# Performance work log

Measured on AMD Instinct MI355X. Metric: run time of the kernel, lower is better.

Reference implementation:

```python
import jax, jax.numpy as jnp
import numpy as np

SIGMA_DIS = 3.0  # from __init__ default sigma_dis=3
PRED_SCALE = 3e-6  # keep sqrt-norms below sigma so max(sigma - d, 0) is not saturated at 0


def setup_inputs() -> dict:
    key = jax.random.key(0)
    k1, k2 = jax.random.split(key)
    C, H, W = 8, 2048, 2048
    K = 32  # number of connected kernel components (labels 1..K, 0 = background)
    pred = jax.random.normal(k1, (C, H, W), dtype=jnp.float32) * PRED_SCALE
    kernel_labels = jax.random.randint(k2, (H, W), 0, K + 1, dtype=jnp.int32)
    regions_mask = jnp.ones((H, W), dtype=bool)  # unused by the original forward
    return {
        "pred_similarities": pred,
        "regions_mask": regions_mask,
        "kernel_labels": kernel_labels,
        "num_kernel": K,
    }


def _l_dis(pred, labels_flat, num_kernel, sigma):
    # pred: [C, H, W]; labels_flat: [H*W] int, values in 0..num_kernel (0 = background).
    C = pred.shape[0]
    flat = pred.reshape(C, -1).T  # [P, C]
    # Per-kernel, per-channel masked sums (the Gk broadcast values): S[k, c]
    S = jax.ops.segment_sum(flat, labels_flat, num_segments=num_kernel + 1)  # [K+1, C]
    # Per-kernel pixel counts N[k]
    N = jax.ops.segment_sum(jnp.ones_like(labels_flat, dtype=pred.dtype),
                            labels_flat, num_segments=num_kernel + 1)  # [K+1]
    # Gk_i has value S[i,c] on kernel i's pixels and 0 elsewhere; supports of distinct
    # kernels are disjoint, so ||Gk_i - Gk_j||_F^2 = N[i]*sum_c S[i,c]^2 + N[j]*sum_c S[j,c]^2.
    A = (N * jnp.sum(S * S, axis=1))[1:]  # [K], drop background label 0
    pair_sq = A[:, None] + A[None, :]  # [K, K]
    D = jnp.maximum(sigma - jnp.sqrt(pair_sq), 0.0)
    term = jnp.log(D * D + 1.0)
    upper = jnp.triu(jnp.ones((num_kernel, num_kernel), dtype=bool), k=1)  # i<j pairs
    L = jnp.sum(jnp.where(upper, term, 0.0))
    scale = (num_kernel - 1) / num_kernel  # 1.0/num_kernel * (num_kernel - 1)
    return L * jnp.asarray(scale, pred.dtype)


def reference(pred_similarities, regions_mask, kernel_labels, num_kernel):
    # regions_mask is accepted but unused, matching the original forward.
    labels_flat = kernel_labels.reshape(-1)
    return _l_dis(pred_similarities, labels_flat, num_kernel, SIGMA_DIS)
```

## Files before the change

kernel.cpp:

```cpp
#include <hip/hip_runtime.h>
#include <hip/hip_bf16.h>
#include <math.h>


typedef __attribute__((ext_vector_type(8))) short short8;
typedef __attribute__((ext_vector_type(4))) float f32x4;

constexpr int NSEGF = 32;
constexpr int RPS   = 9;
constexpr int NROWS = NSEGF * RPS;
constexpr int BLK   = 256;
constexpr int WPB   = 4;
constexpr int NBLK  = 1024;
constexpr int NWAVES= NBLK * WPB;
constexpr int TPX   = 128;
constexpr int L1BLK = 32;
constexpr int SLABS = NBLK / L1BLK;
constexpr int L1BASE   = 1024;
constexpr int PARTBASE = 16384;

#define SCHED_FENCE asm volatile("" ::: "memory")
#define WAITVM(n)   asm volatile("s_waitcnt vmcnt(" #n ")" ::: "memory")

typedef __attribute__((address_space(1))) void A1v;
typedef __attribute__((address_space(3))) void A3v;

__device__ __forceinline__ void gload16(const void* g, void* l) {
  __builtin_amdgcn_global_load_lds((const A1v*)g, (A3v*)l, 16, 0, 0);
}

__device__ __forceinline__ short f2bf(float f) {
  return (short)__bfloat16_as_ushort(__float2bfloat16(f));
}

__device__ __forceinline__ float wave_sum64(float x) {
  int t;
  t = __builtin_amdgcn_update_dpp(0, __float_as_int(x), 0x111, 0xf, 0xf, true); x += __int_as_float(t);
  t = __builtin_amdgcn_update_dpp(0, __float_as_int(x), 0x112, 0xf, 0xf, true); x += __int_as_float(t);
  t = __builtin_amdgcn_update_dpp(0, __float_as_int(x), 0x114, 0xf, 0xf, true); x += __int_as_float(t);
  t = __builtin_amdgcn_update_dpp(0, __float_as_int(x), 0x118, 0xf, 0xf, true); x += __int_as_float(t);
  t = __builtin_amdgcn_update_dpp(0, __float_as_int(x), 0x142, 0xf, 0xf, true); x += __int_as_float(t);
  t = __builtin_amdgcn_update_dpp(0, __float_as_int(x), 0x143, 0xf, 0xf, true); x += __int_as_float(t);
  return x;
}

__device__ __forceinline__ void stage_pred(const float* __restrict__ pred,
                                           float* predbuf,
                                           size_t px0, int lane, size_t P) {
#pragma unroll
  for (int i = 0; i < 4; ++i) {
    const int c   = 2 * i + (lane >> 5);
    const int swb = (((lane & 31) * 16) ^ ((c & 7) << 4));
    gload16(pred + (size_t)c * P + px0 + (swb >> 2), predbuf + i * 256);
  }
}

#define LABLOAD(L0,L1,L2,L3,L4,L5,L6,L7, px0)                                  \
  {                                                                            \
    const int* lg_ = lab + (px0) + quad * 8;                                   \
    L0 = *(const int4*)(lg_ +  0);  L1 = *(const int4*)(lg_ +  4);             \
    L2 = *(const int4*)(lg_ + 32);  L3 = *(const int4*)(lg_ + 36);             \
    L4 = *(const int4*)(lg_ + 64);  L5 = *(const int4*)(lg_ + 68);             \
    L6 = *(const int4*)(lg_ + 96);  L7 = *(const int4*)(lg_ + 100);            \
  }

__device__ __forceinline__ void comp_step(const int4 la, const int4 lc,
                                          const char* prow, int b0, bool isch,
                                          short8 Bconst, int ms0, int ms1,
                                          f32x4& acc0, f32x4& acc1) {
  const short ONE = (short)0x3F80;
  short8 A0, A1, B;
  A0[0] = (la.x == ms0) ? ONE : (short)0;
  A0[1] = (la.y == ms0) ? ONE : (short)0;
  A0[2] = (la.z == ms0) ? ONE : (short)0;
  A0[3] = (la.w == ms0) ? ONE : (short)0;
  A0[4] = (lc.x == ms0) ? ONE : (short)0;
  A0[5] = (lc.y == ms0) ? ONE : (short)0;
  A0[6] = (lc.z == ms0) ? ONE : (short)0;
  A0[7] = (lc.w == ms0) ? ONE : (short)0;
  A1[0] = (la.x == ms1) ? ONE : (short)0;
  A1[1] = (la.y == ms1) ? ONE : (short)0;
  A1[2] = (la.z == ms1) ? ONE : (short)0;
  A1[3] = (la.w == ms1) ? ONE : (short)0;
  A1[4] = (lc.x == ms1) ? ONE : (short)0;
  A1[5] = (lc.y == ms1) ? ONE : (short)0;
  A1[6] = (lc.z == ms1) ? ONE : (short)0;
  A1[7] = (lc.w == ms1) ? ONE : (short)0;
  if (isch) {
    const float4 x = *(const float4*)(prow + b0);
    const float4 y = *(const float4*)(prow + (b0 ^ 16));
    B[0] = f2bf(x.x); B[1] = f2bf(x.y); B[2] = f2bf(x.z); B[3] = f2bf(x.w);
    B[4] = f2bf(y.x); B[5] = f2bf(y.y); B[6] = f2bf(y.z); B[7] = f2bf(y.w);
  } else {
    B = Bconst;
  }
  acc0 = __builtin_amdgcn_mfma_f32_16x16x32_bf16(A0, B, acc0, 0, 0, 0);
  acc1 = __builtin_amdgcn_mfma_f32_16x16x32_bf16(A1, B, acc1, 0, 0, 0);
}

#define COMPUTE_TILE(pbuf)                                                     \
  {                                                                            \
    const char* prow_ = (const char*)((pbuf) + (colq & 7) * TPX);              \
    const int swz_ = ((colq & 7) << 4);                                        \
    comp_step(l0, l1, prow_, (0 * 128 + quad * 32) ^ swz_, isch, Bconst,       \
              ms0, ms1, acc0, acc1);                                           \
    comp_step(l2, l3, prow_, (1 * 128 + quad * 32) ^ swz_, isch, Bconst,       \
              ms0, ms1, acc0, acc1);                                           \
    comp_step(l4, l5, prow_, (2 * 128 + quad * 32) ^ swz_, isch, Bconst,       \
              ms0, ms1, acc0, acc1);                                           \
    comp_step(l6, l7, prow_, (3 * 128 + quad * 32) ^ swz_, isch, Bconst,       \
              ms0, ms1, acc0, acc1);                                           \
  }

__global__ __launch_bounds__(BLK, 4)
void seg_mfma(const float* __restrict__ pred,
              const int*   __restrict__ lab,
              float*       __restrict__ ws,
              int P) {
  __shared__ __align__(16) float predL[WPB][2][8 * TPX];

  const int tid  = threadIdx.x;
  const int wid  = tid >> 6;
  const int lane = tid & 63;
  const int colq = lane & 15;
  const int quad = lane >> 4;
  const int ms0  = colq + 1;
  const int ms1  = colq + 17;
  const bool isch = (colq < 8);

  const int bs = (blockIdx.x & 7) * (NBLK / 8) + (blockIdx.x >> 3);
  const int gw = bs * WPB + wid;

  const int spt = (P / TPX) / NWAVES;
  const size_t px00 = (size_t)gw * spt * TPX;

  f32x4 acc0 = {0.f, 0.f, 0.f, 0.f};
  f32x4 acc1 = {0.f, 0.f, 0.f, 0.f};

  short8 Bconst;
  {
    const short v = (colq == 8) ? (short)0x3F80 : (short)0;
#pragma unroll
    for (int i = 0; i < 8; ++i) Bconst[i] = v;
  }

  float* pb0 = &predL[wid][0][0];
  float* pb1 = &predL[wid][1][0];

  int4 l0, l1, l2, l3, l4, l5, l6, l7;

  LABLOAD(l0, l1, l2, l3, l4, l5, l6, l7, px00)
  stage_pred(pred, pb0, px00, lane, (size_t)P);
  stage_pred(pred, pb1, px00 + TPX, lane, (size_t)P);

  for (int t = 0; t < spt; ++t) {
    if (t < spt - 1) { WAITVM(4); } else { WAITVM(0); }
    const float* pb = (t & 1) ? pb1 : pb0;
    COMPUTE_TILE(pb)
    SCHED_FENCE;
    if (t + 1 < spt) {
      LABLOAD(l0, l1, l2, l3, l4, l5, l6, l7, px00 + (size_t)(t + 1) * TPX)
      if (t + 2 < spt)
        stage_pred(pred, (t & 1) ? pb1 : pb0,
                   px00 + (size_t)(t + 2) * TPX, lane, (size_t)P);
    }
  }

  float* redw = &predL[wid][0][0];
  SCHED_FENCE;
  if (colq < RPS) {
#pragma unroll
    for (int r = 0; r < 4; ++r)
      redw[(quad * 4 + r) * RPS + colq] = acc0[r];
#pragma unroll
    for (int r = 0; r < 4; ++r)
      redw[(16 + quad * 4 + r) * RPS + colq] = acc1[r];
  }
  __syncthreads();
  for (int v = tid; v < NROWS; v += BLK) {
    float s = 0.f;
#pragma unroll
    for (int w = 0; w < WPB; ++w) s += predL[w][0][v];
    ws[PARTBASE + (size_t)blockIdx.x * NROWS + v] = s;
  }
}

__global__ __launch_bounds__(256)
void reduce1(float* __restrict__ ws) {
  const int b = blockIdx.x;
  for (int v = threadIdx.x; v < NROWS; v += 256) {
    float s = 0.f;
#pragma unroll 4
    for (int i = 0; i < SLABS; ++i)
      s += ws[PARTBASE + (size_t)(b * SLABS + i) * NROWS + v];
    ws[L1BASE + (size_t)v * L1BLK + b] = s;
  }
}

__global__ __launch_bounds__(BLK)
void seg_gen(const float* __restrict__ pred,
             const int*   __restrict__ lab,
             float*       __restrict__ ws,
             int P, int C) {
  __shared__ float bins[(NSEGF + 1) * RPS];
  const int tid = threadIdx.x;
  for (int i = tid; i < (NSEGF + 1) * RPS; i += BLK) bins[i] = 0.f;
  __syncthreads();
  const int stride = gridDim.x * BLK;
  const int Cc = C < 8 ? C : 8;
  for (int p = blockIdx.x * BLK + tid; p < P; p += stride) {
    int lb = lab[p]; if (lb < 0) lb = 0; if (lb > NSEGF) lb = NSEGF;
    const int o = lb * RPS;
    unsafeAtomicAdd(&bins[o + 8], 1.f);
    for (int c = 0; c < Cc; ++c)
      unsafeAtomicAdd(&bins[o + c], pred[(size_t)c * P + p]);
  }
  __syncthreads();
  for (int i = tid; i < NROWS; i += BLK)
    ws[PARTBASE + (size_t)blockIdx.x * NROWS + i] = bins[RPS + i];
}

__global__ __launch_bounds__(256)
void finish_kernel(const float* __restrict__ ws,
                   const int*   __restrict__ nkp,
                   float*       __restrict__ out,
                   int C) {
  __shared__ float sfin[NROWS];
  __shared__ float sA[NSEGF + 1];
  __shared__ float wsum[4];
  int K = *nkp; if (K > NSEGF) K = NSEGF;
  const int tid = threadIdx.x;
  const int Cc = C < 8 ? C : 8;

  for (int v = tid; v < NROWS; v += 256) {
    const float* r = ws + L1BASE + (size_t)v * L1BLK;
    float s = 0.f;
#pragma unroll
    for (int b = 0; b < L1BLK; ++b) s += r[b];
    sfin[v] = s;
  }
  __syncthreads();
  for (int k = 1 + tid; k <= K; k += 256) {
    float s2 = 0.f;
    for (int c = 0; c < Cc; ++c) {
      const float v = sfin[(k - 1) * RPS + c];
      s2 = fmaf(v, v, s2);
    }
    sA[k] = sfin[(k - 1) * RPS + 8] * s2;
  }
  __syncthreads();

  const int npairs = K * (K - 1) / 2;
  float accv = 0.f;
  for (int idx = tid; idx < npairs; idx += 256) {
    int i = 1, rem = idx;
    while (rem >= K - i) { rem -= K - i; ++i; }
    const int j = i + 1 + rem;
    const float ps = sA[i] + sA[j];
    const float d  = fmaxf(3.0f - sqrtf(ps), 0.f);
    accv += logf(fmaf(d, d, 1.f));
  }
  accv = wave_sum64(accv);
  if ((tid & 63) == 63) wsum[tid >> 6] = accv;
  __syncthreads();
  if (tid == 0)
    out[0] = (wsum[0] + wsum[1] + wsum[2] + wsum[3]) * (float)(K - 1) / (float)K;
}

extern "C" void kernel_launch(void* const* d_in, const int* in_sizes, int n_in,
                              void* d_out, int out_size, void* d_ws, size_t ws_size,
                              hipStream_t stream) {
  const float* pred = (const float*)d_in[0];
  const int*   lab  = (const int*)d_in[2];
  const int*   nkp  = (const int*)d_in[3];
  float*       out  = (float*)d_out;
  float*       ws   = (float*)d_ws;

  const int P = in_sizes[2];
  const int C = in_sizes[0] / P;

  const size_t need = (size_t)(PARTBASE + (size_t)NBLK * NROWS) * sizeof(float);
  const int spt = (P / TPX) / NWAVES;
  const bool fast = (C == 8) && (P % (TPX * NWAVES)) == 0 && spt >= 2 &&
                    ws_size >= need;

  if (fast) {
    seg_mfma<<<NBLK, BLK, 0, stream>>>(pred, lab, ws, P);
  } else {
    seg_gen<<<NBLK, BLK, 0, stream>>>(pred, lab, ws, P, C);
  }
  reduce1<<<L1BLK, 256, 0, stream>>>(ws);
  finish_kernel<<<1, 256, 0, stream>>>(ws, nkp, out, C);
}
```

Measured before the change: 41.75 us.

## Stage label and pred tiles cooperatively per block with block-level double buffering

```diff
diff --git a/kernel.cpp b/kernel.cpp
--- a/kernel.cpp
+++ b/kernel.cpp
@@ -12,8 +12,7 @@
 constexpr int BLK   = 256;
 constexpr int WPB   = 4;
 constexpr int NBLK  = 1024;
-constexpr int NWAVES= NBLK * WPB;
-constexpr int TPX   = 128;
+constexpr int TPX   = 512;
 constexpr int L1BLK = 32;
 constexpr int SLABS = NBLK / L1BLK;
 constexpr int L1BASE   = 1024;
@@ -44,25 +43,25 @@
   return x;
 }
 
-__device__ __forceinline__ void stage_pred(const float* __restrict__ pred,
-                                           float* predbuf,
-                                           size_t px0, int lane, size_t P) {
-#pragma unroll
-  for (int i = 0; i < 4; ++i) {
-    const int c   = 2 * i + (lane >> 5);
-    const int swb = (((lane & 31) * 16) ^ ((c & 7) << 4));
-    gload16(pred + (size_t)c * P + px0 + (swb >> 2), predbuf + i * 256);
-  }
-}
-
-#define LABLOAD(L0,L1,L2,L3,L4,L5,L6,L7, px0)                                  \
-  {                                                                            \
-    const int* lg_ = lab + (px0) + quad * 8;                                   \
-    L0 = *(const int4*)(lg_ +  0);  L1 = *(const int4*)(lg_ +  4);             \
-    L2 = *(const int4*)(lg_ + 32);  L3 = *(const int4*)(lg_ + 36);             \
-    L4 = *(const int4*)(lg_ + 64);  L5 = *(const int4*)(lg_ + 68);             \
-    L6 = *(const int4*)(lg_ + 96);  L7 = *(const int4*)(lg_ + 100);            \
-  }
+__device__ __forceinline__ void stage_tile(const float* __restrict__ pred,
+                                           const int*   __restrict__ lab,
+                                           float* predbuf, int* labbuf,
+                                           size_t px0, int wid, int lane,
+                                           size_t P) {
+  const int swo = lane * 16;
+#pragma unroll
+  for (int j = 0; j < 2; ++j) {
+    const int c = 2 * wid + j;
+    const int swb = swo ^ ((c & 7) << 4);
+#pragma unroll
+    for (int i = 0; i < 2; ++i) {
+      gload16(pred + (size_t)c * P + px0 + i * 256 + (swb >> 2),
+              predbuf + c * TPX + i * 256);
+    }
+  }
+  if (wid < 2)
+    gload16(lab + px0 + wid * 256 + lane * 4, labbuf + wid * 256);
+}
 
 __device__ __forceinline__ void comp_step(const int4 la, const int4 lc,
                                           const char* prow, int b0, bool isch,
@@ -98,17 +97,23 @@
   acc1 = __builtin_amdgcn_mfma_f32_16x16x32_bf16(A1, B, acc1, 0, 0, 0);
 }
 
-#define COMPUTE_TILE(pbuf)                                                     \
+#define COMPUTE_TILE(pbuf, lbuf)                                               \
   {                                                                            \
-    const char* prow_ = (const char*)((pbuf) + (colq & 7) * TPX);              \
-    const int swz_ = ((colq & 7) << 4);                                        \
-    comp_step(l0, l1, prow_, (0 * 128 + quad * 32) ^ swz_, isch, Bconst,       \
-              ms0, ms1, acc0, acc1);                                           \
-    comp_step(l2, l3, prow_, (1 * 128 + quad * 32) ^ swz_, isch, Bconst,       \
-              ms0, ms1, acc0, acc1);                                           \
-    comp_step(l4, l5, prow_, (2 * 128 + quad * 32) ^ swz_, isch, Bconst,       \
-              ms0, ms1, acc0, acc1);                                           \
-    comp_step(l6, l7, prow_, (3 * 128 + quad * 32) ^ swz_, isch, Bconst,       \
+    const int c_ = colq & 7;                                                   \
+    const char* prow_ = (const char*)((pbuf) + c_ * TPX);                      \
+    const int* lb_ = (lbuf) + wid * 128 + quad * 8;                            \
+    const int swz_ = (c_ << 4);                                                \
+    comp_step(*(const int4*)(lb_ +  0), *(const int4*)(lb_ +  4), prow_,       \
+              (wid * 512 + 0 * 128 + quad * 32) ^ swz_, isch, Bconst,          \
+              ms0, ms1, acc0, acc1);                                           \
+    comp_step(*(const int4*)(lb_ + 32), *(const int4*)(lb_ + 36), prow_,       \
+              (wid * 512 + 1 * 128 + quad * 32) ^ swz_, isch, Bconst,          \
+              ms0, ms1, acc0, acc1);                                           \
+    comp_step(*(const int4*)(lb_ + 64), *(const int4*)(lb_ + 68), prow_,       \
+              (wid * 512 + 2 * 128 + quad * 32) ^ swz_, isch, Bconst,          \
+              ms0, ms1, acc0, acc1);                                           \
+    comp_step(*(const int4*)(lb_ + 96), *(const int4*)(lb_ + 100), prow_,      \
+              (wid * 512 + 3 * 128 + quad * 32) ^ swz_, isch, Bconst,          \
               ms0, ms1, acc0, acc1);                                           \
   }
 
@@ -117,7 +122,8 @@
               const int*   __restrict__ lab,
               float*       __restrict__ ws,
               int P) {
-  __shared__ __align__(16) float predL[WPB][2][8 * TPX];
+  __shared__ __align__(16) float predL[2][8 * TPX];
+  __shared__ __align__(16) int   labL[2][TPX];
 
   const int tid  = threadIdx.x;
   const int wid  = tid >> 6;
@@ -129,10 +135,9 @@
   const bool isch = (colq < 8);
 
   const int bs = (blockIdx.x & 7) * (NBLK / 8) + (blockIdx.x >> 3);
-  const int gw = bs * WPB + wid;
-
-  const int spt = (P / TPX) / NWAVES;
-  const size_t px00 = (size_t)gw * spt * TPX;
+
+  const int spt = (P / TPX) / NBLK;
+  const size_t px00 = (size_t)bs * spt * TPX;
 
   f32x4 acc0 = {0.f, 0.f, 0.f, 0.f};
   f32x4 acc1 = {0.f, 0.f, 0.f, 0.f};
@@ -144,30 +149,29 @@
     for (int i = 0; i < 8; ++i) Bconst[i] = v;
   }
 
-  float* pb0 = &predL[wid][0][0];
-  float* pb1 = &predL[wid][1][0];
-
-  int4 l0, l1, l2, l3, l4, l5, l6, l7;
-
-  LABLOAD(l0, l1, l2, l3, l4, l5, l6, l7, px00)
-  stage_pred(pred, pb0, px00, lane, (size_t)P);
-  stage_pred(pred, pb1, px00 + TPX, lane, (size_t)P);
+  stage_tile(pred, lab, &predL[0][0], &labL[0][0], px00,       wid, lane, (size_t)P);
+  stage_tile(pred, lab, &predL[1][0], &labL[1][0], px00 + TPX, wid, lane, (size_t)P);
 
   for (int t = 0; t < spt; ++t) {
-    if (t < spt - 1) { WAITVM(4); } else { WAITVM(0); }
-    const float* pb = (t & 1) ? pb1 : pb0;
-    COMPUTE_TILE(pb)
-    SCHED_FENCE;
-    if (t + 1 < spt) {
-      LABLOAD(l0, l1, l2, l3, l4, l5, l6, l7, px00 + (size_t)(t + 1) * TPX)
-      if (t + 2 < spt)
-        stage_pred(pred, (t & 1) ? pb1 : pb0,
-                   px00 + (size_t)(t + 2) * TPX, lane, (size_t)P);
-    }
-  }
-
-  float* redw = &predL[wid][0][0];
-  SCHED_FENCE;
+    if (t < spt - 1) {
+      if (wid < 2) { WAITVM(5); } else { WAITVM(4); }
+    } else {
+      WAITVM(0);
+    }
+    __syncthreads();
+    const float* pb = (t & 1) ? &predL[1][0] : &predL[0][0];
+    const int*   lb = (t & 1) ? &labL[1][0] : &labL[0][0];
+    COMPUTE_TILE(pb, lb)
+    __syncthreads();
+    if (t + 2 < spt) {
+      stage_tile(pred, lab, (t & 1) ? &predL[1][0] : &predL[0][0],
+                 (t & 1) ? &labL[1][0] : &labL[0][0],
+                 px00 + (size_t)(t + 2) * TPX, wid, lane, (size_t)P);
+    }
+  }
+
+  __syncthreads();
+  float* redw = &predL[0][0] + wid * NROWS;
   if (colq < RPS) {
 #pragma unroll
     for (int r = 0; r < 4; ++r)
@@ -180,7 +184,7 @@
   for (int v = tid; v < NROWS; v += BLK) {
     float s = 0.f;
 #pragma unroll
-    for (int w = 0; w < WPB; ++w) s += predL[w][0][v];
+    for (int w = 0; w < WPB; ++w) s += predL[0][w * NROWS + v];
     ws[PARTBASE + (size_t)blockIdx.x * NROWS + v] = s;
   }
 }
@@ -280,8 +284,8 @@
   const int C = in_sizes[0] / P;
 
   const size_t need = (size_t)(PARTBASE + (size_t)NBLK * NROWS) * sizeof(float);
-  const int spt = (P / TPX) / NWAVES;
-  const bool fast = (C == 8) && (P % (TPX * NWAVES)) == 0 && spt >= 2 &&
+  const int spt = (P / TPX) / NBLK;
+  const bool fast = (C == 8) && (P % (TPX * NBLK)) == 0 && spt >= 2 &&
                     ws_size >= need;
 
   if (fast) {
```

Result: slower. 52.48 us (+25.7%).
